# Performance work log

Hardware: AMD Instinct MI355X
Metric: run time of the kernel (lower is better)

Reference implementation:

```python
import jax, jax.numpy as jnp
import numpy as np

N_NODES = 100000
N_EDGES = 3200000


def sage_conv(x, src, dst, Wl, bl, Wr, n_nodes):
    # PyG SAGEConv: out = lin_l(mean_{j in N(i)} x_j) + lin_r(x_i)
    msgs = x[src]                                            # [E, d]
    agg = jax.ops.segment_sum(msgs, dst, num_segments=n_nodes)
    cnt = jax.ops.segment_sum(jnp.ones((src.shape[0],), x.dtype), dst,
                              num_segments=n_nodes)
    mean = agg / jnp.maximum(cnt, 1.0)[:, None]
    return mean @ Wl.T + bl + x @ Wr.T


def setup_inputs() -> dict:
    key = jax.random.key(0)
    ks = jax.random.split(key, 9)
    x = jax.random.normal(ks[0], (N_NODES, 6), dtype=jnp.float32)
    edge_index = jax.random.randint(ks[1], (2, N_EDGES), 0, N_NODES, dtype=jnp.int32)
    def glorot(k, shape):
        fan_in = shape[1]
        return jax.random.normal(k, shape, dtype=jnp.float32) / np.sqrt(fan_in)
    return {
        "x": x,
        "edge_index": edge_index,
        "W1l": glorot(ks[2], (12, 6)), "b1": jnp.zeros((12,), jnp.float32),
        "W1r": glorot(ks[3], (12, 6)),
        "W2l": glorot(ks[4], (24, 12)), "b2": jnp.zeros((24,), jnp.float32),
        "W2r": glorot(ks[5], (24, 12)),
        "W3l": glorot(ks[6], (6, 24)), "b3": jnp.zeros((6,), jnp.float32),
        "W3r": glorot(ks[7], (6, 24)),
    }


def reference(x, edge_index, W1l, b1, W1r, W2l, b2, W2r, W3l, b3, W3r):
    src, dst = edge_index[0], edge_index[1]
    h = jax.nn.relu(sage_conv(x, src, dst, W1l, b1, W1r, N_NODES))
    h = jax.nn.relu(sage_conv(h, src, dst, W2l, b2, W2r, N_NODES))
    z = sage_conv(h, src, dst, W3l, b3, W3r, N_NODES)          # [N, 6] encoding
    return z
```

## Files before the change

kernel.cpp:

```cpp
#include <hip/hip_runtime.h>
#include <hip/hip_fp16.h>


#define BSHIFT 9
#define BMASK  511
#define NBMAX  256
#define PART_EDGES 4096
#define BCAP   18000

#define NTL(p) __builtin_nontemporal_load(p)

__device__ __forceinline__ unsigned h2u(__half2 h) { return *reinterpret_cast<unsigned*>(&h); }
__device__ __forceinline__ __half2 u2h(unsigned u) { return *reinterpret_cast<__half2*>(&u); }

__device__ __forceinline__ __half2 red32(__half2 v) {
    int x;
    x = __builtin_amdgcn_update_dpp(0, (int)h2u(v), 0x128, 0xf, 0xf, true);
    v = __hadd2(v, u2h((unsigned)x));
    x = __builtin_amdgcn_update_dpp(0, (int)h2u(v), 0x124, 0xf, 0xf, true);
    v = __hadd2(v, u2h((unsigned)x));
    x = __builtin_amdgcn_update_dpp(0, (int)h2u(v), 0x122, 0xf, 0xf, true);
    v = __hadd2(v, u2h((unsigned)x));
    x = __builtin_amdgcn_update_dpp(0, (int)h2u(v), 0x121, 0xf, 0xf, true);
    v = __hadd2(v, u2h((unsigned)x));
    v = __hadd2(v, u2h(__shfl_xor(h2u(v), 16, 64)));
    return v;
}

__global__ void __launch_bounds__(256)
prep_kernel(const float* __restrict__ x, __half* __restrict__ xh,
            __half* __restrict__ h1, __half* __restrict__ z3lh,
            int* __restrict__ bcur, int n, int nb) {
    if (blockIdx.x == 0) {
        if (threadIdx.x < nb) bcur[threadIdx.x] = threadIdx.x * BCAP;
        if (threadIdx.x < 16) h1[(size_t)n * 16 + threadIdx.x] = __float2half(0.f);
        if (threadIdx.x < 8)  z3lh[(size_t)n * 8 + threadIdx.x] = __float2half(0.f);
    }
    int tid = blockIdx.x * blockDim.x + threadIdx.x;
    if (tid >= (n + 1) * 8) return;
    int i = tid >> 3, f = tid & 7;
    xh[tid] = __float2half((i < n && f < 6) ? x[i * 6 + f] : 0.f);
}

__global__ void __launch_bounds__(256)
partition_kernel(const int* __restrict__ src, const int* __restrict__ dst,
                 int* __restrict__ bcur, unsigned* __restrict__ pairs,
                 int E, int nb) {
    __shared__ int hcnt[NBMAX];
    __shared__ int hbase[NBMAX];
    __shared__ int lofs[NBMAX];
    __shared__ int ssc[256];
    __shared__ unsigned sorted[PART_EDGES];
    __shared__ int gpos[PART_EDGES];

    int lo = blockIdx.x * PART_EDGES;
    int hi = min(E, lo + PART_EDGES);
    int cnt = hi - lo;
    int t = threadIdx.x;

    for (int i = t; i < NBMAX; i += 256) hcnt[i] = 0;
    __syncthreads();

    int myd[16]; unsigned mys[16];
#pragma unroll
    for (int k = 0; k < 16; k++) {
        int i = lo + t + k * 256;
        if (i < hi) { myd[k] = NTL(dst + i); mys[k] = (unsigned)NTL(src + i); }
        else myd[k] = -1;
    }
#pragma unroll
    for (int k = 0; k < 16; k++)
        if (myd[k] >= 0) atomicAdd(&hcnt[myd[k] >> BSHIFT], 1);
    __syncthreads();

    int c = (t < nb) ? hcnt[t] : 0;
    if (t < nb) hbase[t] = c ? atomicAdd(&bcur[t], c) : 0;
    ssc[t] = c;
    __syncthreads();
    for (int off = 1; off < 256; off <<= 1) {
        int x = (t >= off) ? ssc[t - off] : 0;
        __syncthreads();
        ssc[t] += x;
        __syncthreads();
    }
    if (t < nb) { lofs[t] = ssc[t] - c; hcnt[t] = ssc[t] - c; }
    __syncthreads();

#pragma unroll
    for (int k = 0; k < 16; k++) {
        if (myd[k] >= 0) {
            int d = myd[k];
            int b = d >> BSHIFT;
            int r = atomicAdd(&hcnt[b], 1);
            sorted[r] = (mys[k] << BSHIFT) | (unsigned)(d & BMASK);
            gpos[r] = hbase[b] + (r - lofs[b]);
        }
    }
    __syncthreads();

    for (int i = t; i < cnt; i += 256)
        pairs[gpos[i]] = sorted[i];
}

__global__ void __launch_bounds__(1024)
csr_build(const unsigned* __restrict__ pairs,
          const int* __restrict__ bcur,
          int* __restrict__ deg, int* __restrict__ offsets,
          int* __restrict__ ssrc, int n) {
    __shared__ int ldeg[512];
    __shared__ int lcur[512];
    __shared__ int ssc[512];
    int b = blockIdx.x;
    int base = b * BCAP;
    int cnt = bcur[b] - base;
    int t = threadIdx.x;
    if (t < 512) ldeg[t] = 0;
    __syncthreads();
    for (int i = t; i < cnt; i += 1024)
        atomicAdd(&ldeg[NTL(pairs + base + i) & BMASK], 1);
    __syncthreads();
    if (t < 512) ssc[t] = ldeg[t];
    __syncthreads();
    for (int off = 1; off < 512; off <<= 1) {
        int x = (t >= off && t < 512) ? ssc[t - off] : 0;
        __syncthreads();
        if (t < 512) ssc[t] += x;
        __syncthreads();
    }
    if (t < 512) {
        int excl = ssc[t] - ldeg[t];
        lcur[t] = excl;
        int node = (b << BSHIFT) + t;
        if (node < n) { offsets[node] = base + excl; deg[node] = ldeg[t]; }
    }
    __syncthreads();
    for (int i = t; i < cnt; i += 1024) {
        unsigned p = NTL(pairs + base + i);
        int loc = p & BMASK;
        int pos = atomicAdd(&lcur[loc], 1);
        ssrc[base + pos] = (int)(p >> BSHIFT);
    }
}

__global__ void __launch_bounds__(256)
sage_layer1(const __half* __restrict__ xh,
            const int* __restrict__ offsets,
            const int* __restrict__ deg,
            const int* __restrict__ ssrc,
            const float* __restrict__ Wl,
            const float* __restrict__ bb,
            const float* __restrict__ Wr,
            __half* __restrict__ h1, int n) {
    __shared__ __half2 sWl2[36], sWr2[36];
    __shared__ float sb[12];
    int t = threadIdx.x;
    if (t < 36) {
        int r = t / 3, k = t % 3;
        sWl2[t] = __halves2half2(__float2half(Wl[r * 6 + 2 * k]),
                                 __float2half(Wl[r * 6 + 2 * k + 1]));
        sWr2[t] = __halves2half2(__float2half(Wr[r * 6 + 2 * k]),
                                 __float2half(Wr[r * 6 + 2 * k + 1]));
    }
    if (t < 12) sb[t] = bb[t];
    __syncthreads();

    int wid = (blockIdx.x * blockDim.x + threadIdx.x) >> 6;
    int nwaves = (gridDim.x * blockDim.x) >> 6;
    int wl = threadIdx.x & 63;
    int lane = wl & 31;
    int sub = wl >> 5;

    int r = (lane < 12) ? lane : 0;
    __half2 wl2[3], wr2[3];
#pragma unroll
    for (int k = 0; k < 3; k++) { wl2[k] = sWl2[r * 3 + k]; wr2[k] = sWr2[r * 3 + k]; }
    float bias = sb[r];

    int npairs = (n + 1) >> 1;
    __half2 z2 = __float2half2_rn(0.f);

    int pA = wid, pB = wid + nwaves;
    int nodeA = 2 * pA + sub, nodeB = 2 * pB + sub;
    bool vA = (pA < npairs) && (nodeA < n);
    bool vB = (pB < npairs) && (nodeB < n);
    int offA = vA ? offsets[nodeA] : 0, dgA = vA ? deg[nodeA] : 0;
    int offB = vB ? offsets[nodeB] : 0, dgB = vB ? deg[nodeB] : 0;

    int qa0 = ssrc[offA + lane], qa1 = ssrc[offA + lane + 32];
    int qb0 = ssrc[offB + lane], qb1 = ssrc[offB + lane + 32];
    int sa0 = (lane < dgA) ? qa0 : n;
    int sa1 = (lane + 32 < dgA) ? qa1 : n;
    int sb0_ = (lane < dgB) ? qb0 : n;
    int sb1_ = (lane + 32 < dgB) ? qb1 : n;
    uint4 ra0 = *reinterpret_cast<const uint4*>(xh + (size_t)sa0 * 8);
    uint4 ra1 = *reinterpret_cast<const uint4*>(xh + (size_t)sa1 * 8);
    uint4 rb0 = *reinterpret_cast<const uint4*>(xh + (size_t)sb0_ * 8);
    uint4 rb1 = *reinterpret_cast<const uint4*>(xh + (size_t)sb1_ * 8);

    __half2 aA[3], aB[3];
    aA[0] = __hadd2(u2h(ra0.x), u2h(ra1.x));
    aA[1] = __hadd2(u2h(ra0.y), u2h(ra1.y));
    aA[2] = __hadd2(u2h(ra0.z), u2h(ra1.z));
    aB[0] = __hadd2(u2h(rb0.x), u2h(rb1.x));
    aB[1] = __hadd2(u2h(rb0.y), u2h(rb1.y));
    aB[2] = __hadd2(u2h(rb0.z), u2h(rb1.z));

    int m = max(dgA, dgB);
    for (int e = lane + 64; e < m; e += 32) {
        int qa = ssrc[offA + e];
        int qb = ssrc[offB + e];
        int sa = (e < dgA) ? qa : n;
        int sbx = (e < dgB) ? qb : n;
        uint4 ta = *reinterpret_cast<const uint4*>(xh + (size_t)sa * 8);
        uint4 tb = *reinterpret_cast<const uint4*>(xh + (size_t)sbx * 8);
        aA[0] = __hadd2(aA[0], u2h(ta.x)); aA[1] = __hadd2(aA[1], u2h(ta.y));
        aA[2] = __hadd2(aA[2], u2h(ta.z));
        aB[0] = __hadd2(aB[0], u2h(tb.x)); aB[1] = __hadd2(aB[1], u2h(tb.y));
        aB[2] = __hadd2(aB[2], u2h(tb.z));
    }

#pragma unroll
    for (int k = 0; k < 3; k++) { aA[k] = red32(aA[k]); aB[k] = red32(aB[k]); }

    auto epi = [&](int node, int dg, __half2* acc, bool valid) {
        if (valid && lane < 12) {
            uint4 xr = *reinterpret_cast<const uint4*>(xh + (size_t)node * 8);
            __half2 xi2[3] = { u2h(xr.x), u2h(xr.y), u2h(xr.z) };
            __half2 S1 = z2, S2 = z2;
#pragma unroll
            for (int k = 0; k < 3; k++) {
                S1 = __hfma2(acc[k], wl2[k], S1);
                S2 = __hfma2(xi2[k], wr2[k], S2);
            }
            float inv = 1.f / (float)(dg > 0 ? dg : 1);
            float o = (__low2float(S1) + __high2float(S1)) * inv
                    + __low2float(S2) + __high2float(S2) + bias;
            h1[(size_t)node * 16 + lane] = __float2half(fmaxf(o, 0.f));
        }
    };
    epi(nodeA, dgA, aA, vA);
    epi(nodeB, dgB, aB, vB);
}

__global__ void __launch_bounds__(256)
sage_layer2(const __half* __restrict__ h1,
            const int* __restrict__ offsets,
            const int* __restrict__ deg,
            const int* __restrict__ ssrc,
            const float* __restrict__ W2l,
            const float* __restrict__ b2,
            const float* __restrict__ W2r,
            const float* __restrict__ W3l,
            const float* __restrict__ W3r,
            __half* __restrict__ z3lh,
            float* __restrict__ z3r, int n) {
    __shared__ __half2 sW2l2[144], sW2r2[144];
    __shared__ float sW3[300], sb2[24];
    __shared__ __attribute__((aligned(16))) float sh2[4][48];
    int t = threadIdx.x;
    if (t < 144) {
        int r = t / 6, k = t % 6;
        sW2l2[t] = __halves2half2(__float2half(W2l[r * 12 + 2 * k]),
                                  __float2half(W2l[r * 12 + 2 * k + 1]));
        sW2r2[t] = __halves2half2(__float2half(W2r[r * 12 + 2 * k]),
                                  __float2half(W2r[r * 12 + 2 * k + 1]));
        int r3 = t / 24, c3 = t % 24;
        sW3[r3 * 25 + c3] = W3l[t];
        sW3[(r3 + 6) * 25 + c3] = W3r[t];
    }
    if (t < 24) sb2[t] = b2[t];
    __syncthreads();

    int wid = (blockIdx.x * blockDim.x + threadIdx.x) >> 6;
    int nwaves = (gridDim.x * blockDim.x) >> 6;
    int wv = threadIdx.x >> 6;
    int wl = threadIdx.x & 63;
    int lane = wl & 31;
    int sub = wl >> 5;

    int r2 = (lane < 24) ? lane : 0;
    __half2 w2l2[6], w2r2[6];
#pragma unroll
    for (int k = 0; k < 6; k++) { w2l2[k] = sW2l2[r2 * 6 + k]; w2r2[k] = sW2r2[r2 * 6 + k]; }
    float bias = sb2[r2];
    int w3off = (lane < 12) ? lane * 25 : 0;

    int npairs = (n + 1) >> 1;
    __half2 z2 = __float2half2_rn(0.f);

    int p0 = wid, p1 = wid + nwaves;
    int node0 = 2 * p0 + sub, node1 = 2 * p1 + sub;
    bool v0 = (p0 < npairs) && (node0 < n);
    bool v1 = (p1 < npairs) && (node1 < n);
    int off0 = v0 ? offsets[node0] : 0, dg0 = v0 ? deg[node0] : 0;
    int off1 = v1 ? offsets[node1] : 0, dg1 = v1 ? deg[node1] : 0;

    int qa0 = ssrc[off0 + lane], qa1 = ssrc[off0 + lane + 32];
    int qb0 = ssrc[off1 + lane], qb1 = ssrc[off1 + lane + 32];
    int sa0 = (lane < dg0) ? qa0 : n;
    int sa1 = (lane + 32 < dg0) ? qa1 : n;
    int sb0_ = (lane < dg1) ? qb0 : n;
    int sb1_ = (lane + 32 < dg1) ? qb1 : n;
    const char* pa0 = reinterpret_cast<const char*>(h1 + (size_t)sa0 * 16);
    const char* pa1 = reinterpret_cast<const char*>(h1 + (size_t)sa1 * 16);
    const char* pb0 = reinterpret_cast<const char*>(h1 + (size_t)sb0_ * 16);
    const char* pb1 = reinterpret_cast<const char*>(h1 + (size_t)sb1_ * 16);
    uint4 Aa0 = *reinterpret_cast<const uint4*>(pa0);
    uint2 Ba0 = *reinterpret_cast<const uint2*>(pa0 + 16);
    uint4 Aa1 = *reinterpret_cast<const uint4*>(pa1);
    uint2 Ba1 = *reinterpret_cast<const uint2*>(pa1 + 16);
    uint4 Ab0 = *reinterpret_cast<const uint4*>(pb0);
    uint2 Bb0 = *reinterpret_cast<const uint2*>(pb0 + 16);
    uint4 Ab1 = *reinterpret_cast<const uint4*>(pb1);
    uint2 Bb1 = *reinterpret_cast<const uint2*>(pb1 + 16);

    __half2 a0[6], a1[6];
    a0[0] = __hadd2(u2h(Aa0.x), u2h(Aa1.x)); a0[1] = __hadd2(u2h(Aa0.y), u2h(Aa1.y));
    a0[2] = __hadd2(u2h(Aa0.z), u2h(Aa1.z)); a0[3] = __hadd2(u2h(Aa0.w), u2h(Aa1.w));
    a0[4] = __hadd2(u2h(Ba0.x), u2h(Ba1.x)); a0[5] = __hadd2(u2h(Ba0.y), u2h(Ba1.y));
    a1[0] = __hadd2(u2h(Ab0.x), u2h(Ab1.x)); a1[1] = __hadd2(u2h(Ab0.y), u2h(Ab1.y));
    a1[2] = __hadd2(u2h(Ab0.z), u2h(Ab1.z)); a1[3] = __hadd2(u2h(Ab0.w), u2h(Ab1.w));
    a1[4] = __hadd2(u2h(Bb0.x), u2h(Bb1.x)); a1[5] = __hadd2(u2h(Bb0.y), u2h(Bb1.y));

    int m = max(dg0, dg1);
    for (int e = lane + 64; e < m; e += 32) {
        int qa = ssrc[off0 + e];
        int qb = ssrc[off1 + e];
        int sa = (e < dg0) ? qa : n;
        int sbx = (e < dg1) ? qb : n;
        const char* ta = reinterpret_cast<const char*>(h1 + (size_t)sa * 16);
        const char* tb = reinterpret_cast<const char*>(h1 + (size_t)sbx * 16);
        uint4 Ta = *reinterpret_cast<const uint4*>(ta);
        uint2 Ua = *reinterpret_cast<const uint2*>(ta + 16);
        uint4 Tb = *reinterpret_cast<const uint4*>(tb);
        uint2 Ub = *reinterpret_cast<const uint2*>(tb + 16);
        a0[0] = __hadd2(a0[0], u2h(Ta.x)); a0[1] = __hadd2(a0[1], u2h(Ta.y));
        a0[2] = __hadd2(a0[2], u2h(Ta.z)); a0[3] = __hadd2(a0[3], u2h(Ta.w));
        a0[4] = __hadd2(a0[4], u2h(Ua.x)); a0[5] = __hadd2(a0[5], u2h(Ua.y));
        a1[0] = __hadd2(a1[0], u2h(Tb.x)); a1[1] = __hadd2(a1[1], u2h(Tb.y));
        a1[2] = __hadd2(a1[2], u2h(Tb.z)); a1[3] = __hadd2(a1[3], u2h(Tb.w));
        a1[4] = __hadd2(a1[4], u2h(Ub.x)); a1[5] = __hadd2(a1[5], u2h(Ub.y));
    }

    auto finish = [&](int node, int dg, __half2* acc, bool valid) {
#pragma unroll
        for (int k = 0; k < 6; k++) acc[k] = red32(acc[k]);

        float h2v = 0.f;
        if (valid && lane < 24) {
            const char* rp = reinterpret_cast<const char*>(h1 + (size_t)node * 16);
            uint4 x0 = *reinterpret_cast<const uint4*>(rp);
            uint2 x1 = *reinterpret_cast<const uint2*>(rp + 16);
            __half2 xi2[6] = { u2h(x0.x), u2h(x0.y), u2h(x0.z),
                               u2h(x0.w), u2h(x1.x), u2h(x1.y) };
            __half2 S1 = z2, S2 = z2;
#pragma unroll
            for (int k = 0; k < 6; k++) {
                S1 = __hfma2(acc[k], w2l2[k], S1);
                S2 = __hfma2(xi2[k], w2r2[k], S2);
            }
            float inv = 1.f / (float)(dg > 0 ? dg : 1);
            float o = (__low2float(S1) + __high2float(S1)) * inv
                    + __low2float(S2) + __high2float(S2) + bias;
            h2v = fmaxf(o, 0.f);
        }
        if (lane < 24) sh2[wv][sub * 24 + lane] = h2v;
        float z = 0.f;
        if (lane < 12) {
            const float4* hp = reinterpret_cast<const float4*>(sh2[wv] + sub * 24);
#pragma unroll
            for (int k = 0; k < 6; k++) {
                float4 h4 = hp[k];
                float w0 = sW3[w3off + 4 * k],     w1 = sW3[w3off + 4 * k + 1];
                float w2 = sW3[w3off + 4 * k + 2], w3 = sW3[w3off + 4 * k + 3];
                z += h4.x * w0 + h4.y * w1 + h4.z * w2 + h4.w * w3;
            }
        }
        if (valid) {
            if (lane < 6)               z3lh[(size_t)node * 8 + lane] = __float2half(z);
            else if (lane < 8)          z3lh[(size_t)node * 8 + lane] = __float2half(0.f);
            if (lane >= 6 && lane < 12) z3r[(size_t)node * 6 + (lane - 6)] = z;
        }
    };
    finish(node0, dg0, a0, v0);
    finish(node1, dg1, a1, v1);
}

__global__ void __launch_bounds__(256)
sage_layer3(const __half* __restrict__ z3lh,
            const int* __restrict__ offsets,
            const int* __restrict__ deg,
            const int* __restrict__ ssrc,
            const float* __restrict__ b3,
            const float* __restrict__ z3r,
            float* __restrict__ out, int n) {
    int wid = (blockIdx.x * blockDim.x + threadIdx.x) >> 6;
    int nwaves = (gridDim.x * blockDim.x) >> 6;
    int wl = threadIdx.x & 63;
    int lane = wl & 31;
    int sub = wl >> 5;

    float b3v = b3[(lane < 6) ? lane : 0];

    int npairs = (n + 1) >> 1;

    int pA = wid, pB = wid + nwaves;
    int nodeA = 2 * pA + sub, nodeB = 2 * pB + sub;
    bool vA = (pA < npairs) && (nodeA < n);
    bool vB = (pB < npairs) && (nodeB < n);
    int offA = vA ? offsets[nodeA] : 0, dgA = vA ? deg[nodeA] : 0;
    int offB = vB ? offsets[nodeB] : 0, dgB = vB ? deg[nodeB] : 0;

    int qa0 = ssrc[offA + lane], qa1 = ssrc[offA + lane + 32];
    int qb0 = ssrc[offB + lane], qb1 = ssrc[offB + lane + 32];
    int sa0 = (lane < dgA) ? qa0 : n;
    int sa1 = (lane + 32 < dgA) ? qa1 : n;
    int sb0_ = (lane < dgB) ? qb0 : n;
    int sb1_ = (lane + 32 < dgB) ? qb1 : n;
    uint4 ra0 = *reinterpret_cast<const uint4*>(z3lh + (size_t)sa0 * 8);
    uint4 ra1 = *reinterpret_cast<const uint4*>(z3lh + (size_t)sa1 * 8);
    uint4 rb0 = *reinterpret_cast<const uint4*>(z3lh + (size_t)sb0_ * 8);
    uint4 rb1 = *reinterpret_cast<const uint4*>(z3lh + (size_t)sb1_ * 8);

    __half2 aA[3], aB[3];
    aA[0] = __hadd2(u2h(ra0.x), u2h(ra1.x));
    aA[1] = __hadd2(u2h(ra0.y), u2h(ra1.y));
    aA[2] = __hadd2(u2h(ra0.z), u2h(ra1.z));
    aB[0] = __hadd2(u2h(rb0.x), u2h(rb1.x));
    aB[1] = __hadd2(u2h(rb0.y), u2h(rb1.y));
    aB[2] = __hadd2(u2h(rb0.z), u2h(rb1.z));

    int m = max(dgA, dgB);
    for (int e = lane + 64; e < m; e += 32) {
        int qa = ssrc[offA + e];
        int qb = ssrc[offB + e];
        int sa = (e < dgA) ? qa : n;
        int sbx = (e < dgB) ? qb : n;
        uint4 ta = *reinterpret_cast<const uint4*>(z3lh + (size_t)sa * 8);
        uint4 tb = *reinterpret_cast<const uint4*>(z3lh + (size_t)sbx * 8);
        aA[0] = __hadd2(aA[0], u2h(ta.x)); aA[1] = __hadd2(aA[1], u2h(ta.y));
        aA[2] = __hadd2(aA[2], u2h(ta.z));
        aB[0] = __hadd2(aB[0], u2h(tb.x)); aB[1] = __hadd2(aB[1], u2h(tb.y));
        aB[2] = __hadd2(aB[2], u2h(tb.z));
    }

#pragma unroll
    for (int k = 0; k < 3; k++) { aA[k] = red32(aA[k]); aB[k] = red32(aB[k]); }

    auto epi = [&](int node, int dg, __half2* acc, bool valid) {
        if (valid && lane < 6) {
            float fa[6] = { __low2float(acc[0]), __high2float(acc[0]),
                            __low2float(acc[1]), __high2float(acc[1]),
                            __low2float(acc[2]), __high2float(acc[2]) };
            float inv = 1.f / (float)(dg > 0 ? dg : 1);
            out[(size_t)node * 6 + lane] = fa[lane] * inv + b3v
                                         + z3r[(size_t)node * 6 + lane];
        }
    };
    epi(nodeA, dgA, aA, vA);
    epi(nodeB, dgB, aB, vB);
}

extern "C" void kernel_launch(void* const* d_in, const int* in_sizes, int n_in,
                              void* d_out, int out_size, void* d_ws, size_t ws_size,
                              hipStream_t stream) {
    const float* x   = (const float*)d_in[0];
    const int* eidx  = (const int*)d_in[1];
    const float* W1l = (const float*)d_in[2];
    const float* b1  = (const float*)d_in[3];
    const float* W1r = (const float*)d_in[4];
    const float* W2l = (const float*)d_in[5];
    const float* b2  = (const float*)d_in[6];
    const float* W2r = (const float*)d_in[7];
    const float* W3l = (const float*)d_in[8];
    const float* b3  = (const float*)d_in[9];
    const float* W3r = (const float*)d_in[10];

    const int n = in_sizes[0] / 6;
    const int E = in_sizes[1] / 2;
    const int* src = eidx;
    const int* dst = eidx + E;
    const int nb = (n + BMASK) >> BSHIFT;

    char* w = (char*)d_ws;
    auto carve = [&](size_t bytes) {
        char* p = w;
        w += (bytes + 255) & ~(size_t)255;
        return p;
    };
    int*      bcur    = (int*)carve((size_t)NBMAX * 4);
    unsigned* pairs   = (unsigned*)carve((size_t)nb * BCAP * 4);
    int*      ssrc    = (int*)carve((size_t)nb * BCAP * 4 + 256);
    int*      deg     = (int*)carve((size_t)n * 4);
    int*      offsets = (int*)carve((size_t)n * 4);
    __half*   xh      = (__half*)carve((size_t)(n + 1) * 8 * 2);
    __half*   h1      = (__half*)carve((size_t)(n + 1) * 16 * 2);
    __half*   z3lh    = (__half*)carve((size_t)(n + 1) * 8 * 2);
    float*    z3r     = (float*)carve((size_t)n * 6 * 4);

    const int part_blocks = (E + PART_EDGES - 1) / PART_EDGES;
    prep_kernel<<<((n + 1) * 8 + 255) / 256, 256, 0, stream>>>(x, xh, h1, z3lh,
                                                               bcur, n, nb);
    partition_kernel<<<part_blocks, 256, 0, stream>>>(src, dst, bcur, pairs, E, nb);
    csr_build<<<nb, 1024, 0, stream>>>(pairs, bcur, deg, offsets, ssrc, n);

    const int LBLK = 6250;
    sage_layer1<<<LBLK, 256, 0, stream>>>(xh, offsets, deg, ssrc, W1l, b1, W1r, h1, n);
    sage_layer2<<<LBLK, 256, 0, stream>>>(h1, offsets, deg, ssrc,
                                          W2l, b2, W2r, W3l, W3r, z3lh, z3r, n);
    sage_layer3<<<LBLK, 256, 0, stream>>>(z3lh, offsets, deg, ssrc, b3, z3r,
                                          (float*)d_out, n);
}
```

Baseline: 211.4 us.

## Fuse prep into partition, use DPP wave scans, nontemporal CSR loads

```diff
diff --git a/kernel.cpp b/kernel.cpp
--- a/kernel.cpp
+++ b/kernel.cpp
@@ -27,36 +27,51 @@
     return v;
 }
 
+__device__ __forceinline__ int wscan_incl(int x) {
+    x += __builtin_amdgcn_update_dpp(0, x, 0x111, 0xf, 0xf, true);
+    x += __builtin_amdgcn_update_dpp(0, x, 0x112, 0xf, 0xf, true);
+    x += __builtin_amdgcn_update_dpp(0, x, 0x114, 0xf, 0xf, true);
+    x += __builtin_amdgcn_update_dpp(0, x, 0x118, 0xf, 0xf, true);
+    x += __builtin_amdgcn_update_dpp(0, x, 0x142, 0xa, 0xf, true);
+    x += __builtin_amdgcn_update_dpp(0, x, 0x143, 0xc, 0xf, true);
+    return x;
+}
+
 __global__ void __launch_bounds__(256)
-prep_kernel(const float* __restrict__ x, __half* __restrict__ xh,
-            __half* __restrict__ h1, __half* __restrict__ z3lh,
-            int* __restrict__ bcur, int n, int nb) {
-    if (blockIdx.x == 0) {
-        if (threadIdx.x < nb) bcur[threadIdx.x] = threadIdx.x * BCAP;
-        if (threadIdx.x < 16) h1[(size_t)n * 16 + threadIdx.x] = __float2half(0.f);
-        if (threadIdx.x < 8)  z3lh[(size_t)n * 8 + threadIdx.x] = __float2half(0.f);
-    }
-    int tid = blockIdx.x * blockDim.x + threadIdx.x;
-    if (tid >= (n + 1) * 8) return;
-    int i = tid >> 3, f = tid & 7;
-    xh[tid] = __float2half((i < n && f < 6) ? x[i * 6 + f] : 0.f);
-}
-
-__global__ void __launch_bounds__(256)
-partition_kernel(const int* __restrict__ src, const int* __restrict__ dst,
+partition_kernel(const float* __restrict__ x, __half* __restrict__ xh,
+                 __half* __restrict__ h1, __half* __restrict__ z3lh,
+                 const int* __restrict__ src, const int* __restrict__ dst,
                  int* __restrict__ bcur, unsigned* __restrict__ pairs,
-                 int E, int nb) {
+                 int E, int n, int nb) {
     __shared__ int hcnt[NBMAX];
     __shared__ int hbase[NBMAX];
     __shared__ int lofs[NBMAX];
-    __shared__ int ssc[256];
+    __shared__ int wtot[4];
     __shared__ unsigned sorted[PART_EDGES];
     __shared__ int gpos[PART_EDGES];
+
+    int t = threadIdx.x;
+
+    int gid = blockIdx.x * 256 + t;
+    if (gid <= n) {
+        uint4 o = make_uint4(0u, 0u, 0u, 0u);
+        if (gid < n) {
+            const float2* xp = reinterpret_cast<const float2*>(x + (size_t)gid * 6);
+            float2 a = xp[0], b = xp[1], c = xp[2];
+            o.x = h2u(__floats2half2_rn(a.x, a.y));
+            o.y = h2u(__floats2half2_rn(b.x, b.y));
+            o.z = h2u(__floats2half2_rn(c.x, c.y));
+        }
+        *reinterpret_cast<uint4*>(xh + (size_t)gid * 8) = o;
+    }
+    if (blockIdx.x == 0) {
+        if (t < 16) h1[(size_t)n * 16 + t] = __float2half(0.f);
+        if (t < 8)  z3lh[(size_t)n * 8 + t] = __float2half(0.f);
+    }
 
     int lo = blockIdx.x * PART_EDGES;
     int hi = min(E, lo + PART_EDGES);
     int cnt = hi - lo;
-    int t = threadIdx.x;
 
     for (int i = t; i < NBMAX; i += 256) hcnt[i] = 0;
     __syncthreads();
@@ -74,16 +89,16 @@
     __syncthreads();
 
     int c = (t < nb) ? hcnt[t] : 0;
-    if (t < nb) hbase[t] = c ? atomicAdd(&bcur[t], c) : 0;
-    ssc[t] = c;
-    __syncthreads();
-    for (int off = 1; off < 256; off <<= 1) {
-        int x = (t >= off) ? ssc[t - off] : 0;
-        __syncthreads();
-        ssc[t] += x;
-        __syncthreads();
-    }
-    if (t < nb) { lofs[t] = ssc[t] - c; hcnt[t] = ssc[t] - c; }
+    if (t < nb) hbase[t] = c ? (t * BCAP + atomicAdd(&bcur[t], c)) : 0;
+    int sc = wscan_incl(c);
+    if ((t & 63) == 63) wtot[t >> 6] = sc;
+    __syncthreads();
+    int ofs = 0;
+#pragma unroll
+    for (int j = 0; j < 3; j++)
+        if (j < (t >> 6)) ofs += wtot[j];
+    int excl = sc + ofs - c;
+    if (t < nb) { lofs[t] = excl; hcnt[t] = excl; }
     __syncthreads();
 
 #pragma unroll
@@ -109,29 +124,29 @@
           int* __restrict__ ssrc, int n) {
     __shared__ int ldeg[512];
     __shared__ int lcur[512];
-    __shared__ int ssc[512];
+    __shared__ int wtot[8];
     int b = blockIdx.x;
     int base = b * BCAP;
-    int cnt = bcur[b] - base;
+    int cnt = bcur[b];
     int t = threadIdx.x;
     if (t < 512) ldeg[t] = 0;
     __syncthreads();
     for (int i = t; i < cnt; i += 1024)
         atomicAdd(&ldeg[NTL(pairs + base + i) & BMASK], 1);
     __syncthreads();
-    if (t < 512) ssc[t] = ldeg[t];
-    __syncthreads();
-    for (int off = 1; off < 512; off <<= 1) {
-        int x = (t >= off && t < 512) ? ssc[t - off] : 0;
-        __syncthreads();
-        if (t < 512) ssc[t] += x;
-        __syncthreads();
-    }
+    int c = (t < 512) ? ldeg[t] : 0;
+    int sc = wscan_incl(c);
+    if (t < 512 && (t & 63) == 63) wtot[t >> 6] = sc;
+    __syncthreads();
     if (t < 512) {
-        int excl = ssc[t] - ldeg[t];
+        int ofs = 0;
+#pragma unroll
+        for (int j = 0; j < 7; j++)
+            if (j < (t >> 6)) ofs += wtot[j];
+        int excl = sc + ofs - c;
         lcur[t] = excl;
         int node = (b << BSHIFT) + t;
-        if (node < n) { offsets[node] = base + excl; deg[node] = ldeg[t]; }
+        if (node < n) { offsets[node] = base + excl; deg[node] = c; }
     }
     __syncthreads();
     for (int i = t; i < cnt; i += 1024) {
@@ -183,11 +198,11 @@
     int nodeA = 2 * pA + sub, nodeB = 2 * pB + sub;
     bool vA = (pA < npairs) && (nodeA < n);
     bool vB = (pB < npairs) && (nodeB < n);
-    int offA = vA ? offsets[nodeA] : 0, dgA = vA ? deg[nodeA] : 0;
-    int offB = vB ? offsets[nodeB] : 0, dgB = vB ? deg[nodeB] : 0;
-
-    int qa0 = ssrc[offA + lane], qa1 = ssrc[offA + lane + 32];
-    int qb0 = ssrc[offB + lane], qb1 = ssrc[offB + lane + 32];
+    int offA = vA ? NTL(offsets + nodeA) : 0, dgA = vA ? NTL(deg + nodeA) : 0;
+    int offB = vB ? NTL(offsets + nodeB) : 0, dgB = vB ? NTL(deg + nodeB) : 0;
+
+    int qa0 = NTL(ssrc + offA + lane), qa1 = NTL(ssrc + offA + lane + 32);
+    int qb0 = NTL(ssrc + offB + lane), qb1 = NTL(ssrc + offB + lane + 32);
     int sa0 = (lane < dgA) ? qa0 : n;
     int sa1 = (lane + 32 < dgA) ? qa1 : n;
     int sb0_ = (lane < dgB) ? qb0 : n;
@@ -207,8 +222,8 @@
 
     int m = max(dgA, dgB);
     for (int e = lane + 64; e < m; e += 32) {
-        int qa = ssrc[offA + e];
-        int qb = ssrc[offB + e];
+        int qa = NTL(ssrc + offA + e);
+        int qb = NTL(ssrc + offB + e);
         int sa = (e < dgA) ? qa : n;
         int sbx = (e < dgB) ? qb : n;
         uint4 ta = *reinterpret_cast<const uint4*>(xh + (size_t)sa * 8);
@@ -292,11 +307,11 @@
     int node0 = 2 * p0 + sub, node1 = 2 * p1 + sub;
     bool v0 = (p0 < npairs) && (node0 < n);
     bool v1 = (p1 < npairs) && (node1 < n);
-    int off0 = v0 ? offsets[node0] : 0, dg0 = v0 ? deg[node0] : 0;
-    int off1 = v1 ? offsets[node1] : 0, dg1 = v1 ? deg[node1] : 0;
-
-    int qa0 = ssrc[off0 + lane], qa1 = ssrc[off0 + lane + 32];
-    int qb0 = ssrc[off1 + lane], qb1 = ssrc[off1 + lane + 32];
+    int off0 = v0 ? NTL(offsets + node0) : 0, dg0 = v0 ? NTL(deg + node0) : 0;
+    int off1 = v1 ? NTL(offsets + node1) : 0, dg1 = v1 ? NTL(deg + node1) : 0;
+
+    int qa0 = NTL(ssrc + off0 + lane), qa1 = NTL(ssrc + off0 + lane + 32);
+    int qb0 = NTL(ssrc + off1 + lane), qb1 = NTL(ssrc + off1 + lane + 32);
     int sa0 = (lane < dg0) ? qa0 : n;
     int sa1 = (lane + 32 < dg0) ? qa1 : n;
     int sb0_ = (lane < dg1) ? qb0 : n;
@@ -324,8 +339,8 @@
 
     int m = max(dg0, dg1);
     for (int e = lane + 64; e < m; e += 32) {
-        int qa = ssrc[off0 + e];
-        int qb = ssrc[off1 + e];
+        int qa = NTL(ssrc + off0 + e);
+        int qb = NTL(ssrc + off1 + e);
         int sa = (e < dg0) ? qa : n;
         int sbx = (e < dg1) ? qb : n;
         const char* ta = reinterpret_cast<const char*>(h1 + (size_t)sa * 16);
@@ -408,11 +423,11 @@
     int nodeA = 2 * pA + sub, nodeB = 2 * pB + sub;
     bool vA = (pA < npairs) && (nodeA < n);
     bool vB = (pB < npairs) && (nodeB < n);
-    int offA = vA ? offsets[nodeA] : 0, dgA = vA ? deg[nodeA] : 0;
-    int offB = vB ? offsets[nodeB] : 0, dgB = vB ? deg[nodeB] : 0;
-
-    int qa0 = ssrc[offA + lane], qa1 = ssrc[offA + lane + 32];
-    int qb0 = ssrc[offB + lane], qb1 = ssrc[offB + lane + 32];
+    int offA = vA ? NTL(offsets + nodeA) : 0, dgA = vA ? NTL(deg + nodeA) : 0;
+    int offB = vB ? NTL(offsets + nodeB) : 0, dgB = vB ? NTL(deg + nodeB) : 0;
+
+    int qa0 = NTL(ssrc + offA + lane), qa1 = NTL(ssrc + offA + lane + 32);
+    int qb0 = NTL(ssrc + offB + lane), qb1 = NTL(ssrc + offB + lane + 32);
     int sa0 = (lane < dgA) ? qa0 : n;
     int sa1 = (lane + 32 < dgA) ? qa1 : n;
     int sb0_ = (lane < dgB) ? qb0 : n;
@@ -432,8 +447,8 @@
 
     int m = max(dgA, dgB);
     for (int e = lane + 64; e < m; e += 32) {
-        int qa = ssrc[offA + e];
-        int qb = ssrc[offB + e];
+        int qa = NTL(ssrc + offA + e);
+        int qb = NTL(ssrc + offB + e);
         int sa = (e < dgA) ? qa : n;
         int sbx = (e < dgB) ? qb : n;
         uint4 ta = *reinterpret_cast<const uint4*>(z3lh + (size_t)sa * 8);
@@ -454,7 +469,7 @@
                             __low2float(acc[2]), __high2float(acc[2]) };
             float inv = 1.f / (float)(dg > 0 ? dg : 1);
             out[(size_t)node * 6 + lane] = fa[lane] * inv + b3v
-                                         + z3r[(size_t)node * 6 + lane];
+                                         + NTL(z3r + (size_t)node * 6 + lane);
         }
     };
     epi(nodeA, dgA, aA, vA);
@@ -499,9 +514,10 @@
     float*    z3r     = (float*)carve((size_t)n * 6 * 4);
 
     const int part_blocks = (E + PART_EDGES - 1) / PART_EDGES;
-    prep_kernel<<<((n + 1) * 8 + 255) / 256, 256, 0, stream>>>(x, xh, h1, z3lh,
-                                                               bcur, n, nb);
-    partition_kernel<<<part_blocks, 256, 0, stream>>>(src, dst, bcur, pairs, E, nb);
+
+    hipMemsetAsync(bcur, 0, (size_t)NBMAX * 4, stream);
+    partition_kernel<<<part_blocks, 256, 0, stream>>>(x, xh, h1, z3lh,
+                                                      src, dst, bcur, pairs, E, n, nb);
     csr_build<<<nb, 1024, 0, stream>>>(pairs, bcur, deg, offsets, ssrc, n);
 
     const int LBLK = 6250;
```

Result: slower. 222.8 us (+5.4%).
